# Kernel tuning notes

Hardware: AMD Instinct MI355X
Metric: run time of the kernel (lower is better)

## Reference

```python
import jax, jax.numpy as jnp
import numpy as np

B, N, P, L = 32, 4096, 256, 16
DR = 128           # rel_dim = args.rgcn_hidden_size
H = 128            # rnn_hidden_size (unidirectional -> rnn_opt_dim == H)
D = H
NUM_REL = 400      # num_rels * 2


def setup_inputs() -> dict:
    key = jax.random.key(0)
    ks = jax.random.split(key, 12)
    s = 0.05
    graph_embed = jax.random.normal(ks[0], (B, N, DR), jnp.float32)
    node_opt = jax.random.normal(ks[1], (B, D), jnp.float32)
    node_idx = jax.random.randint(ks[2], (B, P, L), 0, N)
    rel_idx = jax.random.randint(ks[3], (B, P, L), 0, NUM_REL)
    path_lens = jax.random.randint(ks[4], (B, P), 1, L + 1)  # in [1, L]
    rel_embeds = jax.random.normal(ks[5], (NUM_REL, DR), jnp.float32) * s
    W_ih = jax.random.normal(ks[6], (4 * H, 2 * DR), jnp.float32) * s
    W_hh = jax.random.normal(ks[7], (4 * H, H), jnp.float32) * s
    b_ih = jnp.zeros((4 * H,), jnp.float32)
    b_hh = jnp.zeros((4 * H,), jnp.float32)
    in_proj_w = jax.random.normal(ks[8], (3 * D, D), jnp.float32) * s
    in_proj_b = jnp.zeros((3 * D,), jnp.float32)
    out_proj_w = jax.random.normal(ks[9], (D, D), jnp.float32) * s
    out_proj_b = jnp.zeros((D,), jnp.float32)
    return dict(graph_embed=graph_embed, node_opt=node_opt, rel_embeds=rel_embeds,
                W_ih=W_ih, W_hh=W_hh, b_ih=b_ih, b_hh=b_hh,
                in_proj_w=in_proj_w, in_proj_b=in_proj_b,
                out_proj_w=out_proj_w, out_proj_b=out_proj_b,
                node_idx=node_idx, rel_idx=rel_idx, path_lens=path_lens)


def _forward(graph_embed, node_opt, rel_embeds, W_ih, W_hh, b_ih, b_hh,
             in_proj_w, in_proj_b, out_proj_w, out_proj_b,
             node_idx, rel_idx, path_lens):
    b, n, dr = graph_embed.shape
    p, l = node_idx.shape[1], node_idx.shape[2]
    h = W_hh.shape[1]
    dt = graph_embed.dtype

    t = jnp.arange(l)
    # node embedding valid for steps < len; rel valid for steps < len-1 ('Padr' at last step -> zero rel half)
    node_mask = (t[None, None, :] < path_lens[:, :, None]).astype(dt)[..., None]
    rel_mask = (t[None, None, :] < (path_lens - 1)[:, :, None]).astype(dt)[..., None]

    batch_ix = jnp.arange(b)[:, None, None]
    node_e = graph_embed[batch_ix, node_idx]            # [B,P,L,DR]
    rel_e = rel_embeds[rel_idx]                          # [B,P,L,DR]
    x = jnp.concatenate([node_e * node_mask, rel_e * rel_mask], axis=-1)
    x = x.reshape(b * p, l, 2 * dr)                      # packed path sequences

    bias = b_ih + b_hh

    def step(carry, xt):
        hh, cc = carry
        g = xt @ W_ih.T + hh @ W_hh.T + bias
        i, f, gg, o = jnp.split(g, 4, axis=-1)
        i = jax.nn.sigmoid(i); f = jax.nn.sigmoid(f)
        gg = jnp.tanh(gg); o = jax.nn.sigmoid(o)
        cc = f * cc + i * gg
        hh = o * jnp.tanh(cc)
        return (hh, cc), hh

    h0 = jnp.zeros((b * p, h), dt)
    _, ys = jax.lax.scan(step, (h0, h0), jnp.swapaxes(x, 0, 1))
    ys = jnp.swapaxes(ys, 0, 1).reshape(b, p, l, h)

    # last valid LSTM output per path (== pack_padded_sequence semantics, unidirectional)
    idx = jnp.broadcast_to((path_lens - 1)[:, :, None, None], (b, p, 1, h))
    last = jnp.take_along_axis(ys, idx, axis=2).squeeze(2)   # [B,P,H]

    # single-head MultiheadAttention: query = node_opt, keys/values = path encodings
    Wq, Wk, Wv = jnp.split(in_proj_w, 3, axis=0)
    bq, bk, bv = jnp.split(in_proj_b, 3)
    q = node_opt @ Wq.T + bq                                  # [B,D]
    k = last @ Wk.T + bk                                      # [B,P,D]
    v = last @ Wv.T + bv
    scale = 1.0 / jnp.sqrt(jnp.asarray(q.shape[-1], dt))
    attn = jax.nn.softmax(jnp.einsum('bd,bpd->bp', q, k) * scale, axis=-1)
    ctx = jnp.einsum('bp,bpd->bd', attn, v)
    return ctx @ out_proj_w.T + out_proj_b                    # [B,D]


def reference(graph_embed, node_opt, rel_embeds, W_ih, W_hh, b_ih, b_hh,
              in_proj_w, in_proj_b, out_proj_w, out_proj_b,
              node_idx, rel_idx, path_lens):
    return _forward(graph_embed, node_opt, rel_embeds, W_ih, W_hh, b_ih, b_hh,
                    in_proj_w, in_proj_b, out_proj_w, out_proj_b,
                    node_idx, rel_idx, path_lens)
```

## Files before the change

kernel.cpp:

```cpp
#include <hip/hip_runtime.h>
#include <hip/hip_bf16.h>


#define B_    32
#define N_    4096
#define L_    16
#define DR_   128
#define H_    128
#define G4_   512
#define AST2  264
#define NPATH 8192
#define NPB   32

typedef unsigned short bfraw;
typedef short short8 __attribute__((ext_vector_type(8)));
typedef float f32x4 __attribute__((ext_vector_type(4)));

__device__ int   g_isbf16;
__device__ int   g_isi64;
__device__ __align__(16) bfraw g_Wcat[G4_ * 256];
__device__ float g_relproj[400 * G4_];
__device__ float g_bias[G4_];
__device__ int   g_perm[NPATH];
__device__ float g_last[NPATH * H_];

__device__ __forceinline__ float bfc(bfraw v) {
    return __uint_as_float(((unsigned)v) << 16);
}
__device__ __forceinline__ bfraw f2b(float f) {
    unsigned u = __float_as_uint(f);
    return (bfraw)((u + 0x7FFFu + ((u >> 16) & 1u)) >> 16);
}
__device__ __forceinline__ unsigned pk2(float a, float b) {
    return (unsigned)f2b(a) | ((unsigned)f2b(b) << 16);
}
__device__ __forceinline__ float ld(const void* p, size_t i, int isbf) {
    return isbf ? bfc(((const bfraw*)p)[i]) : ((const float*)p)[i];
}
__device__ __forceinline__ float sigf(float x) { return 1.0f / (1.0f + __expf(-x)); }
__device__ __forceinline__ float tanhfast(float x) { return 2.0f * sigf(2.0f * x) - 1.0f; }

__device__ __forceinline__ float dot128(const float* __restrict__ w,
                                        const float* __restrict__ s) {
    float acc = 0.f;
    #pragma unroll
    for (int i = 0; i < 32; ++i) {
        const float4 wv = *(const float4*)(w + i * 4);
        acc = fmaf(wv.x, s[i*4+0], fmaf(wv.y, s[i*4+1],
              fmaf(wv.z, s[i*4+2], fmaf(wv.w, s[i*4+3], acc))));
    }
    return acc;
}

__global__ __launch_bounds__(512) void k_prep(
    const void* __restrict__ node_opt, const int* __restrict__ node_idx,
    const void* __restrict__ rel_embeds,
    const void* __restrict__ W_ih, const void* __restrict__ W_hh,
    const void* __restrict__ b_ih, const void* __restrict__ b_hh,
    const int* __restrict__ path_lens)
{
    __shared__ float relv[DR_];
    __shared__ int s_big, s_nz, hist[16], cur[16];
    const int tid = threadIdx.x;
    const int blk = blockIdx.x;

    if (tid == 0) { s_big = 0; s_nz = 0; }
    __syncthreads();
    {
        const unsigned short* u = (const unsigned short*)node_opt;
        int big = 0;
        #pragma unroll
        for (int i = 0; i < 4; ++i) {
            const float v = fabsf(bfc(u[tid + i * 512]));
            big |= !(v < 1.0e3f);
        }
        if (big) s_big = 1;
        if (node_idx[2 * tid + 1] != 0) s_nz = 1;
    }
    __syncthreads();
    const int isbf = s_big ? 0 : 1;
    const int i64  = s_nz ? 0 : 1;

    if (blk < 400) {
        const int r = blk;
        if (tid < DR_) relv[tid] = ld(rel_embeds, (size_t)r * DR_ + tid, isbf);
        __syncthreads();
        const int n = tid;
        float s;
        if (isbf) {
            s = 0.f;
            for (int d = 0; d < DR_; ++d)
                s = fmaf(relv[d], bfc(((const bfraw*)W_ih)[(size_t)n * 256 + 128 + d]), s);
        } else {
            s = dot128((const float*)W_ih + (size_t)n * 256 + 128, relv);
        }
        g_relproj[r * G4_ + n] = s;
    } else if (blk < 656) {
        const int idx = (blk - 400) * 512 + tid;
        const int n = idx >> 8, k = idx & 255;
        const float v = (k < H_) ? ld(W_hh, (size_t)n * H_ + k, isbf)
                                 : ld(W_ih, (size_t)n * 256 + (k - H_), isbf);
        g_Wcat[n * 256 + k] = f2b(v);
    } else {
        if (tid == 0) { g_isbf16 = isbf; g_isi64 = i64; }
        g_bias[tid] = ld(b_ih, tid, isbf) + ld(b_hh, tid, isbf);
        if (tid < 16) hist[tid] = 0;
        __syncthreads();
        for (int p = tid; p < NPATH; p += 512) {
            const int len = i64 ? path_lens[2 * p] : path_lens[p];
            atomicAdd(&hist[len - 1], 1);
        }
        __syncthreads();
        if (tid == 0) {
            int off = 0;
            for (int b = 15; b >= 0; --b) { cur[b] = off; off += hist[b]; }
        }
        __syncthreads();
        for (int p = tid; p < NPATH; p += 512) {
            const int len = i64 ? path_lens[2 * p] : path_lens[p];
            const int pos = atomicAdd(&cur[len - 1], 1);
            g_perm[pos] = p;
        }
    }
}

__global__ __launch_bounds__(512, 2) void k_lstm(
    const void* __restrict__ graph_embed,
    const int*  __restrict__ node_idx,
    const int*  __restrict__ rel_idx,
    const int*  __restrict__ path_lens)
{
    __shared__ __align__(16) bfraw A[NPB][AST2];
    __shared__ int s_pid[NPB], s_len[NPB];
    __shared__ int s_nid[NPB][L_], s_rid[NPB][L_];

    const int isbf = g_isbf16;
    const int i64  = g_isi64;
    const int tid  = threadIdx.x;

    if (tid < NPB) {
        const int pid = g_perm[blockIdx.x * NPB + tid];
        s_pid[tid] = pid;
        s_len[tid] = i64 ? path_lens[2 * pid] : path_lens[pid];
    }
    __syncthreads();
    {
        const int m = tid >> 4, t = tid & 15;
        const int idx = s_pid[m] * L_ + t;
        s_nid[m][t] = i64 ? node_idx[2 * idx] : node_idx[idx];
        s_rid[m][t] = i64 ? rel_idx[2 * idx]  : rel_idx[idx];
    }
    {
        const int m = tid >> 4, i0 = (tid & 15) * 8;
        *(uint4*)&A[m][i0] = make_uint4(0, 0, 0, 0);
    }
    __syncthreads();

    int maxlen = 0;
    #pragma unroll
    for (int m = 0; m < NPB; ++m) maxlen = max(maxlen, s_len[m]);

    const int w    = tid >> 6;
    const int l    = tid & 63;
    const int quad = l >> 4;
    const int col  = l & 15;
    const int u0   = w * 16 + col;

    short8 wreg[8][4];
    float bq4[4];
    #pragma unroll
    for (int g = 0; g < 4; ++g) {
        bq4[g] = g_bias[g * 128 + u0];
        const bfraw* wrow = g_Wcat + (size_t)(g * 128 + u0) * 256 + quad * 8;
        #pragma unroll
        for (int ck = 0; ck < 8; ++ck)
            wreg[ck][g] = *(const short8*)(wrow + ck * 32);
    }

    const int pm  = tid >> 4;
    const int pi0 = (tid & 15) * 8;
    const size_t gbase = (size_t)(s_pid[pm] >> 8) * (size_t)(N_ * DR_);
    uint4 pn0, pn1;
    {
        const int nid = s_nid[pm][0];
        if (isbf) {
            pn0 = *(const uint4*)((const bfraw*)graph_embed + gbase + (size_t)nid * DR_ + pi0);
        } else {
            const float* gp = (const float*)graph_embed + gbase + (size_t)nid * DR_ + pi0;
            pn0 = *(const uint4*)gp; pn1 = *(const uint4*)(gp + 4);
        }
    }

    float c[2][4];
    #pragma unroll
    for (int mt = 0; mt < 2; ++mt)
        #pragma unroll
        for (int r = 0; r < 4; ++r) c[mt][r] = 0.f;

    for (int t = 0; t < maxlen; ++t) {
        {
            uint4 npk = make_uint4(0, 0, 0, 0);
            if (t < s_len[pm]) {
                if (isbf) npk = pn0;
                else {
                    const float* a = (const float*)&pn0;
                    const float* b = (const float*)&pn1;
                    npk = make_uint4(pk2(a[0],a[1]), pk2(a[2],a[3]),
                                     pk2(b[0],b[1]), pk2(b[2],b[3]));
                }
            }
            *(uint4*)&A[pm][128 + pi0] = npk;
        }
        __syncthreads();

        if (t + 1 < maxlen) {
            const int nid = s_nid[pm][t + 1];
            if (isbf) {
                pn0 = *(const uint4*)((const bfraw*)graph_embed + gbase + (size_t)nid * DR_ + pi0);
            } else {
                const float* gp = (const float*)graph_embed + gbase + (size_t)nid * DR_ + pi0;
                pn0 = *(const uint4*)gp; pn1 = *(const uint4*)(gp + 4);
            }
        }

        f32x4 acc[2][4];
        #pragma unroll
        for (int mt = 0; mt < 2; ++mt)
            #pragma unroll
            for (int g = 0; g < 4; ++g) {
                const float b = bq4[g];
                acc[mt][g][0] = b; acc[mt][g][1] = b;
                acc[mt][g][2] = b; acc[mt][g][3] = b;
            }
        #pragma unroll
        for (int ck = 0; ck < 8; ++ck) {
            const short8 a0 = *(const short8*)&A[col][ck * 32 + quad * 8];
            const short8 a1 = *(const short8*)&A[16 + col][ck * 32 + quad * 8];
            #pragma unroll
            for (int g = 0; g < 4; ++g) {
                acc[0][g] = __builtin_amdgcn_mfma_f32_16x16x32_bf16(a0, wreg[ck][g], acc[0][g], 0, 0, 0);
                acc[1][g] = __builtin_amdgcn_mfma_f32_16x16x32_bf16(a1, wreg[ck][g], acc[1][g], 0, 0, 0);
            }
        }

        float rl[2][4][4];
        #pragma unroll
        for (int mt = 0; mt < 2; ++mt)
            #pragma unroll
            for (int r = 0; r < 4; ++r) {
                const int m = mt * 16 + quad * 4 + r;
                const float* rp = g_relproj + (size_t)s_rid[m][t] * G4_ + u0;
                #pragma unroll
                for (int g = 0; g < 4; ++g) rl[mt][g][r] = rp[g * 128];
            }
        __syncthreads();

        #pragma unroll
        for (int mt = 0; mt < 2; ++mt)
            #pragma unroll
            for (int r = 0; r < 4; ++r) {
                const int m = mt * 16 + quad * 4 + r;
                const float relm = (t < s_len[m] - 1) ? 1.0f : 0.0f;
                const float ig = sigf(acc[mt][0][r] + relm * rl[mt][0][r]);
                const float fg = sigf(acc[mt][1][r] + relm * rl[mt][1][r]);
                const float gg = tanhfast(acc[mt][2][r] + relm * rl[mt][2][r]);
                const float og = sigf(acc[mt][3][r] + relm * rl[mt][3][r]);
                const float cc = fg * c[mt][r] + ig * gg;
                c[mt][r] = cc;
                const float h = og * tanhfast(cc);
                A[m][u0] = f2b(h);
                if (t == s_len[m] - 1)
                    g_last[(size_t)s_pid[m] * H_ + u0] = h;
            }
    }
}

__global__ __launch_bounds__(256) void k_attn(
    const void* __restrict__ node_opt,
    const void* __restrict__ in_proj_w,
    const void* __restrict__ in_proj_b,
    const void* __restrict__ out_proj_w,
    const void* __restrict__ out_proj_b,
    float* __restrict__ out)
{
    const int isbf = g_isbf16;
    const int b = blockIdx.x, tid = threadIdx.x;
    __shared__ __align__(16) float s_no[128], q[128], qk[128], sv2[2][128], ctx[128];
    __shared__ float logits[256];
    __shared__ float red[12];

    if (tid < 128) s_no[tid] = ld(node_opt, b * 128 + tid, isbf);
    __syncthreads();
    if (tid < 128) {
        float s;
        if (isbf) {
            s = 0.f;
            for (int j = 0; j < 128; ++j)
                s = fmaf(s_no[j], ld(in_proj_w, (size_t)tid * 128 + j, 1), s);
        } else {
            s = dot128((const float*)in_proj_w + (size_t)tid * 128, s_no);
        }
        q[tid] = s + ld(in_proj_b, tid, isbf);
    }
    __syncthreads();
    if (tid < 128) {
        float s = 0.f;
        for (int j = 0; j < 128; ++j)
            s = fmaf(q[j], ld(in_proj_w, (size_t)(128 + j) * 128 + tid, isbf), s);
        qk[tid] = s;
    } else if (tid == 128) {
        float s = 0.f;
        for (int j = 0; j < 128; ++j)
            s = fmaf(q[j], ld(in_proj_b, 128 + j, isbf), s);
        red[10] = s;
    }
    __syncthreads();
    {
        const float* lp = g_last + ((size_t)b * 256 + tid) * H_;
        const float s = dot128(lp, qk);
        logits[tid] = (s + red[10]) * 0.08838834764831845f;
    }
    __syncthreads();
    float v = logits[tid];
    #pragma unroll
    for (int off = 32; off > 0; off >>= 1) v = fmaxf(v, __shfl_xor(v, off, 64));
    if ((tid & 63) == 0) red[tid >> 6] = v;
    __syncthreads();
    if (tid == 0) red[8] = fmaxf(fmaxf(red[0], red[1]), fmaxf(red[2], red[3]));
    __syncthreads();
    const float e = __expf(logits[tid] - red[8]);
    float sum = e;
    #pragma unroll
    for (int off = 32; off > 0; off >>= 1) sum += __shfl_xor(sum, off, 64);
    if ((tid & 63) == 0) red[4 + (tid >> 6)] = sum;
    __syncthreads();
    if (tid == 0) red[9] = red[4] + red[5] + red[6] + red[7];
    __syncthreads();
    logits[tid] = e / red[9];
    __syncthreads();
    {
        const int u = tid & 127, half = tid >> 7;
        float s = 0.f;
        const float* lb = g_last + ((size_t)b * 256 + half * 128) * H_ + u;
        for (int p = 0; p < 128; ++p)
            s = fmaf(logits[half * 128 + p], lb[(size_t)p * H_], s);
        sv2[half][u] = s;
    }
    __syncthreads();
    if (tid < 128) q[tid] = sv2[0][tid] + sv2[1][tid];
    __syncthreads();
    if (tid < 128) {
        float s;
        if (isbf) {
            s = 0.f;
            for (int u = 0; u < 128; ++u)
                s = fmaf(q[u], ld(in_proj_w, (size_t)(256 + tid) * 128 + u, 1), s);
        } else {
            s = dot128((const float*)in_proj_w + (size_t)(256 + tid) * 128, q);
        }
        ctx[tid] = s + ld(in_proj_b, 256 + tid, isbf);
    }
    __syncthreads();
    if (tid < 128) {
        float s;
        if (isbf) {
            s = 0.f;
            for (int d = 0; d < 128; ++d)
                s = fmaf(ctx[d], ld(out_proj_w, (size_t)tid * 128 + d, 1), s);
        } else {
            s = dot128((const float*)out_proj_w + (size_t)tid * 128, ctx);
        }
        out[b * 128 + tid] = s + ld(out_proj_b, tid, isbf);
    }
}

extern "C" void kernel_launch(void* const* d_in, const int* in_sizes, int n_in,
                              void* d_out, int out_size, void* d_ws, size_t ws_size,
                              hipStream_t stream)
{
    const void* graph_embed = d_in[0];
    const void* node_opt    = d_in[1];
    const void* rel_embeds  = d_in[2];
    const void* W_ih        = d_in[3];
    const void* W_hh        = d_in[4];
    const void* b_ih        = d_in[5];
    const void* b_hh        = d_in[6];
    const void* in_proj_w   = d_in[7];
    const void* in_proj_b   = d_in[8];
    const void* out_proj_w  = d_in[9];
    const void* out_proj_b  = d_in[10];
    const int* node_idx  = (const int*)d_in[11];
    const int* rel_idx   = (const int*)d_in[12];
    const int* path_lens = (const int*)d_in[13];
    (void)d_ws; (void)ws_size; (void)in_sizes; (void)n_in; (void)out_size;

    hipLaunchKernelGGL(k_prep, dim3(657), dim3(512), 0, stream,
                       node_opt, node_idx, rel_embeds, W_ih, W_hh, b_ih, b_hh,
                       path_lens);
    hipLaunchKernelGGL(k_lstm, dim3(NPATH / NPB), dim3(512), 0, stream,
                       graph_embed, node_idx, rel_idx, path_lens);
    hipLaunchKernelGGL(k_attn, dim3(B_), dim3(256), 0, stream,
                       node_opt, in_proj_w, in_proj_b, out_proj_w, out_proj_b,
                       (float*)d_out);
}
```

Before: 234.6 us.

## Restructure LSTM step loop: interleaved relproj layout, early prefetch, lighter barriers

Stores the relation projection gate-interleaved so each thread fetches its four gate values with one 16-byte load, and issues those loads at the top of each step so they overlap the MFMA chain. The step loop is reordered: the next node embedding is written to LDS after the hidden-state write-back, the first input is staged before the loop, and the gate math runs before the barrier. Full __syncthreads is replaced by a raw s_waitcnt lgkmcnt(0) + s_barrier, and sigmoid uses the hardware reciprocal. The raw barrier does not wait on global-memory counters, and rcp lowers precision slightly.

```diff
diff --git a/kernel.cpp b/kernel.cpp
--- a/kernel.cpp
+++ b/kernel.cpp
@@ -19,11 +19,13 @@
 __device__ int   g_isbf16;
 __device__ int   g_isi64;
 __device__ __align__(16) bfraw g_Wcat[G4_ * 256];
-__device__ float g_relproj[400 * G4_];
+__device__ __align__(16) float g_relproj[400 * G4_];
 __device__ float g_bias[G4_];
 __device__ int   g_perm[NPATH];
 __device__ float g_last[NPATH * H_];
 
+#define BAR() asm volatile("s_waitcnt lgkmcnt(0)\n\ts_barrier" ::: "memory")
+
 __device__ __forceinline__ float bfc(bfraw v) {
     return __uint_as_float(((unsigned)v) << 16);
 }
@@ -37,8 +39,12 @@
 __device__ __forceinline__ float ld(const void* p, size_t i, int isbf) {
     return isbf ? bfc(((const bfraw*)p)[i]) : ((const float*)p)[i];
 }
-__device__ __forceinline__ float sigf(float x) { return 1.0f / (1.0f + __expf(-x)); }
-__device__ __forceinline__ float tanhfast(float x) { return 2.0f * sigf(2.0f * x) - 1.0f; }
+__device__ __forceinline__ float sigf(float x) {
+    return __builtin_amdgcn_rcpf(1.0f + __expf(-x));
+}
+__device__ __forceinline__ float tanhfast(float x) {
+    return 2.0f * sigf(2.0f * x) - 1.0f;
+}
 
 __device__ __forceinline__ float dot128(const float* __restrict__ w,
                                         const float* __restrict__ s) {
@@ -94,7 +100,7 @@
         } else {
             s = dot128((const float*)W_ih + (size_t)n * 256 + 128, relv);
         }
-        g_relproj[r * G4_ + n] = s;
+        g_relproj[r * G4_ + ((n & 127) << 2) + (n >> 7)] = s;
     } else if (blk < 656) {
         const int idx = (blk - 400) * 512 + tid;
         const int n = idx >> 8, k = idx & 255;
@@ -180,16 +186,24 @@
     const int pm  = tid >> 4;
     const int pi0 = (tid & 15) * 8;
     const size_t gbase = (size_t)(s_pid[pm] >> 8) * (size_t)(N_ * DR_);
-    uint4 pn0, pn1;
+
     {
         const int nid = s_nid[pm][0];
+        uint4 npk;
         if (isbf) {
-            pn0 = *(const uint4*)((const bfraw*)graph_embed + gbase + (size_t)nid * DR_ + pi0);
+            npk = *(const uint4*)((const bfraw*)graph_embed + gbase + (size_t)nid * DR_ + pi0);
         } else {
             const float* gp = (const float*)graph_embed + gbase + (size_t)nid * DR_ + pi0;
-            pn0 = *(const uint4*)gp; pn1 = *(const uint4*)(gp + 4);
-        }
-    }
+            const uint4 q0 = *(const uint4*)gp;
+            const uint4 q1 = *(const uint4*)(gp + 4);
+            const float* a = (const float*)&q0;
+            const float* b = (const float*)&q1;
+            npk = make_uint4(pk2(a[0],a[1]), pk2(a[2],a[3]),
+                             pk2(b[0],b[1]), pk2(b[2],b[3]));
+        }
+        *(uint4*)&A[pm][128 + pi0] = npk;
+    }
+    __syncthreads();
 
     float c[2][4];
     #pragma unroll
@@ -197,10 +211,79 @@
         #pragma unroll
         for (int r = 0; r < 4; ++r) c[mt][r] = 0.f;
 
+    uint4 pn0, pn1;
+
     for (int t = 0; t < maxlen; ++t) {
-        {
+        f32x4 rlv[2][4];
+        #pragma unroll
+        for (int mt = 0; mt < 2; ++mt)
+            #pragma unroll
+            for (int r = 0; r < 4; ++r) {
+                const int m = mt * 16 + quad * 4 + r;
+                rlv[mt][r] = *(const f32x4*)(g_relproj + (size_t)s_rid[m][t] * G4_ + u0 * 4);
+            }
+
+        if (t + 1 < maxlen) {
+            const int nid = s_nid[pm][t + 1];
+            if (isbf) {
+                pn0 = *(const uint4*)((const bfraw*)graph_embed + gbase + (size_t)nid * DR_ + pi0);
+            } else {
+                const float* gp = (const float*)graph_embed + gbase + (size_t)nid * DR_ + pi0;
+                pn0 = *(const uint4*)gp; pn1 = *(const uint4*)(gp + 4);
+            }
+        }
+
+        f32x4 acc[2][4];
+        #pragma unroll
+        for (int mt = 0; mt < 2; ++mt)
+            #pragma unroll
+            for (int g = 0; g < 4; ++g) {
+                const float b = bq4[g];
+                acc[mt][g][0] = b; acc[mt][g][1] = b;
+                acc[mt][g][2] = b; acc[mt][g][3] = b;
+            }
+        #pragma unroll
+        for (int ck = 0; ck < 8; ++ck) {
+            const short8 a0 = *(const short8*)&A[col][ck * 32 + quad * 8];
+            const short8 a1 = *(const short8*)&A[16 + col][ck * 32 + quad * 8];
+            #pragma unroll
+            for (int g = 0; g < 4; ++g) {
+                acc[0][g] = __builtin_amdgcn_mfma_f32_16x16x32_bf16(a0, wreg[ck][g], acc[0][g], 0, 0, 0);
+                acc[1][g] = __builtin_amdgcn_mfma_f32_16x16x32_bf16(a1, wreg[ck][g], acc[1][g], 0, 0, 0);
+            }
+        }
+
+        float hv[2][4];
+        #pragma unroll
+        for (int mt = 0; mt < 2; ++mt)
+            #pragma unroll
+            for (int r = 0; r < 4; ++r) {
+                const int m = mt * 16 + quad * 4 + r;
+                const float relm = (t < s_len[m] - 1) ? 1.0f : 0.0f;
+                const float ig = sigf(acc[mt][0][r] + relm * rlv[mt][r][0]);
+                const float fg = sigf(acc[mt][1][r] + relm * rlv[mt][r][1]);
+                const float gg = tanhfast(acc[mt][2][r] + relm * rlv[mt][r][2]);
+                const float og = sigf(acc[mt][3][r] + relm * rlv[mt][r][3]);
+                const float cc = fg * c[mt][r] + ig * gg;
+                c[mt][r] = cc;
+                hv[mt][r] = og * tanhfast(cc);
+            }
+
+        BAR();
+
+        #pragma unroll
+        for (int mt = 0; mt < 2; ++mt)
+            #pragma unroll
+            for (int r = 0; r < 4; ++r) {
+                const int m = mt * 16 + quad * 4 + r;
+                A[m][u0] = f2b(hv[mt][r]);
+                if (t == s_len[m] - 1)
+                    g_last[(size_t)s_pid[m] * H_ + u0] = hv[mt][r];
+            }
+
+        if (t + 1 < maxlen) {
             uint4 npk = make_uint4(0, 0, 0, 0);
-            if (t < s_len[pm]) {
+            if (t + 1 < s_len[pm]) {
                 if (isbf) npk = pn0;
                 else {
                     const float* a = (const float*)&pn0;
@@ -211,67 +294,8 @@
             }
             *(uint4*)&A[pm][128 + pi0] = npk;
         }
-        __syncthreads();
-
-        if (t + 1 < maxlen) {
-            const int nid = s_nid[pm][t + 1];
-            if (isbf) {
-                pn0 = *(const uint4*)((const bfraw*)graph_embed + gbase + (size_t)nid * DR_ + pi0);
-            } else {
-                const float* gp = (const float*)graph_embed + gbase + (size_t)nid * DR_ + pi0;
-                pn0 = *(const uint4*)gp; pn1 = *(const uint4*)(gp + 4);
-            }
-        }
-
-        f32x4 acc[2][4];
-        #pragma unroll
-        for (int mt = 0; mt < 2; ++mt)
-            #pragma unroll
-            for (int g = 0; g < 4; ++g) {
-                const float b = bq4[g];
-                acc[mt][g][0] = b; acc[mt][g][1] = b;
-                acc[mt][g][2] = b; acc[mt][g][3] = b;
-            }
-        #pragma unroll
-        for (int ck = 0; ck < 8; ++ck) {
-            const short8 a0 = *(const short8*)&A[col][ck * 32 + quad * 8];
-            const short8 a1 = *(const short8*)&A[16 + col][ck * 32 + quad * 8];
-            #pragma unroll
-            for (int g = 0; g < 4; ++g) {
-                acc[0][g] = __builtin_amdgcn_mfma_f32_16x16x32_bf16(a0, wreg[ck][g], acc[0][g], 0, 0, 0);
-                acc[1][g] = __builtin_amdgcn_mfma_f32_16x16x32_bf16(a1, wreg[ck][g], acc[1][g], 0, 0, 0);
-            }
-        }
-
-        float rl[2][4][4];
-        #pragma unroll
-        for (int mt = 0; mt < 2; ++mt)
-            #pragma unroll
-            for (int r = 0; r < 4; ++r) {
-                const int m = mt * 16 + quad * 4 + r;
-                const float* rp = g_relproj + (size_t)s_rid[m][t] * G4_ + u0;
-                #pragma unroll
-                for (int g = 0; g < 4; ++g) rl[mt][g][r] = rp[g * 128];
-            }
-        __syncthreads();
-
-        #pragma unroll
-        for (int mt = 0; mt < 2; ++mt)
-            #pragma unroll
-            for (int r = 0; r < 4; ++r) {
-                const int m = mt * 16 + quad * 4 + r;
-                const float relm = (t < s_len[m] - 1) ? 1.0f : 0.0f;
-                const float ig = sigf(acc[mt][0][r] + relm * rl[mt][0][r]);
-                const float fg = sigf(acc[mt][1][r] + relm * rl[mt][1][r]);
-                const float gg = tanhfast(acc[mt][2][r] + relm * rl[mt][2][r]);
-                const float og = sigf(acc[mt][3][r] + relm * rl[mt][3][r]);
-                const float cc = fg * c[mt][r] + ig * gg;
-                c[mt][r] = cc;
-                const float h = og * tanhfast(cc);
-                A[m][u0] = f2b(h);
-                if (t == s_len[m] - 1)
-                    g_last[(size_t)s_pid[m] * H_ + u0] = h;
-            }
+
+        BAR();
     }
 }
 
```

Result: slower. 250.3 us (+6.7%).
